# Performance work log

Hardware: AMD Instinct MI355X
Metric: run time of the kernel (lower is better)

Reference implementation:

```python
import jax, jax.numpy as jnp
import numpy as np

V, E, H, L, B, S = 32000, 256, 512, 2, 128, 512


def _lstm_step(x, h, c, w_ih, w_hh, b_ih, b_hh):
    # PyTorch gate order: i, f, g, o
    gates = x @ w_ih.T + b_ih + h @ w_hh.T + b_hh
    i, f, g, o = jnp.split(gates, 4, axis=-1)
    c2 = jax.nn.sigmoid(f) * c + jax.nn.sigmoid(i) * jnp.tanh(g)
    h2 = jax.nn.sigmoid(o) * jnp.tanh(c2)
    return h2, c2


def setup_inputs() -> dict:
    key = jax.random.key(0)
    ks = jax.random.split(key, 16)
    s = 0.05
    d = {}
    d["dec_input"] = jax.random.randint(ks[0], (B,), 0, V)
    d["hidden"] = jax.random.normal(ks[1], (L, B, H), jnp.float32)
    d["cell"] = jax.random.normal(ks[2], (L, B, H), jnp.float32)
    d["encoder_outputs"] = jax.random.normal(ks[3], (S, B, H), jnp.float32)
    d["emb"] = jax.random.normal(ks[4], (V, E), jnp.float32) * s
    d["attn_w"] = jax.random.normal(ks[5], (1, 2 * H), jnp.float32) * s
    d["attn_b"] = jnp.zeros((1,), jnp.float32)
    d["w_ih0"] = jax.random.normal(ks[6], (4 * H, E + H), jnp.float32) * s
    d["w_hh0"] = jax.random.normal(ks[7], (4 * H, H), jnp.float32) * s
    d["b_ih0"] = jnp.zeros((4 * H,), jnp.float32)
    d["b_hh0"] = jnp.zeros((4 * H,), jnp.float32)
    d["w_ih1"] = jax.random.normal(ks[8], (4 * H, H), jnp.float32) * s
    d["w_hh1"] = jax.random.normal(ks[9], (4 * H, H), jnp.float32) * s
    d["b_ih1"] = jnp.zeros((4 * H,), jnp.float32)
    d["b_hh1"] = jnp.zeros((4 * H,), jnp.float32)
    d["fc_w"] = jax.random.normal(ks[10], (V, H), jnp.float32) * s
    d["fc_b"] = jnp.zeros((V,), jnp.float32)
    return d


def reference(dec_input, hidden, cell, encoder_outputs, emb, attn_w, attn_b,
              w_ih0, w_hh0, b_ih0, b_hh0, w_ih1, w_hh1, b_ih1, b_hh1,
              fc_w, fc_b):
    # embedded: [B, E]  (dropout p=0 -> identity)
    embedded = emb[dec_input]
    # Bahdanau-style additive scoring using FIRST-layer hidden (as in source)
    h0 = hidden[0]                                   # [B, H]
    w_enc, w_hid = attn_w[0, :H], attn_w[0, H:]      # split linear over concat
    # logits[b,s] = enc[s,b]@w_enc + h0[b]@w_hid + b
    logits = jnp.einsum('sbh,h->bs', encoder_outputs, w_enc) \
        + (h0 @ w_hid)[:, None] + attn_b[0]          # [B, S]
    alpha = jax.nn.softmax(logits, axis=1)           # softmax over src positions
    # context = sum_s alpha[b,s] * enc[s,b,:]  (avoids repeat_interleave blowup)
    context = jnp.einsum('bs,sbh->bh', alpha, encoder_outputs)  # [B, H]
    x = jnp.concatenate([context, embedded], axis=1)            # [B, H+E]
    # single-timestep 2-layer LSTM
    h_0, c_0 = _lstm_step(x, hidden[0], cell[0], w_ih0, w_hh0, b_ih0, b_hh0)
    h_1, c_1 = _lstm_step(h_0, hidden[1], cell[1], w_ih1, w_hh1, b_ih1, b_hh1)
    new_hidden = jnp.stack([h_0, h_1])
    new_cell = jnp.stack([c_0, c_1])
    prediction = h_1 @ fc_w.T + fc_b                 # [B, V]
    return prediction, new_hidden, new_cell
```

## Files before the change

### kernel.cpp

```cpp
#include <hip/hip_runtime.h>
#include <hip/hip_bf16.h>
#include <math.h>

constexpr int NV = 32000;
constexpr int NE = 256;
constexpr int NH = 512;
constexpr int NB = 128;
constexpr int NS = 512;
constexpr int NX = NH + NE;
constexpr int NSC = 8;

typedef __attribute__((ext_vector_type(8))) short short8;
typedef __attribute__((ext_vector_type(4))) short short4v;
typedef __attribute__((ext_vector_type(4))) float f32x4;

constexpr size_t OFF_PCTX  = 0;
constexpr size_t OFF_PML   = OFF_PCTX  + (size_t)NB*NSC*NH;
constexpr size_t OFF_XBF   = OFF_PML   + (size_t)NB*NSC*2;
constexpr size_t OFF_H0NBF = OFF_XBF   + 49152;
constexpr size_t OFF_H1NBF = OFF_H0NBF + 32768;
constexpr size_t OFF_H0BFI = OFF_H1NBF + 32768;
constexpr size_t OFF_H1BFI = OFF_H0BFI + 32768;

constexpr size_t OUT_HID  = (size_t)NB * NV;
constexpr size_t OUT_CELL = OUT_HID + 2ull * NB * NH;

__device__ inline float sigf(float x) { return 1.0f / (1.0f + expf(-x)); }
__device__ inline short bf16s(float x) {
  __hip_bfloat16 h = __float2bfloat16(x);
  return *reinterpret_cast<short*>(&h);
}

__global__ __launch_bounds__(256) void attn_partial_k(
    const float* __restrict__ enc, const float* __restrict__ attn_w,
    float* __restrict__ pctx, float* __restrict__ pml) {
  const int sc = blockIdx.x, b = blockIdx.y;
  const int wv = threadIdx.x >> 6, lane = threadIdx.x & 63;
  const f32x4 wa = *reinterpret_cast<const f32x4*>(attn_w + lane * 4);
  const f32x4 wb = *reinterpret_cast<const f32x4*>(attn_w + 256 + lane * 4);
  float m0 = -INFINITY, l0 = 0.f, m1 = -INFINITY, l1 = 0.f;
  f32x4 a00 = {}, a01 = {}, a10 = {}, a11 = {};
  const float* base = enc + ((size_t)(sc * 64 + wv) * NB + b) * NH;
  for (int i = 0; i < 8; ++i) {
    const float* r0 = base + (size_t)(i * 4) * NB * NH;
    const float* r1 = base + (size_t)((i + 8) * 4) * NB * NH;
    f32x4 e00 = *reinterpret_cast<const f32x4*>(r0 + lane * 4);
    f32x4 e01 = *reinterpret_cast<const f32x4*>(r0 + 256 + lane * 4);
    f32x4 e10 = *reinterpret_cast<const f32x4*>(r1 + lane * 4);
    f32x4 e11 = *reinterpret_cast<const f32x4*>(r1 + 256 + lane * 4);
    float d0 = e00.x * wa.x + e00.y * wa.y + e00.z * wa.z + e00.w * wa.w
             + e01.x * wb.x + e01.y * wb.y + e01.z * wb.z + e01.w * wb.w;
    float d1 = e10.x * wa.x + e10.y * wa.y + e10.z * wa.z + e10.w * wa.w
             + e11.x * wb.x + e11.y * wb.y + e11.z * wb.z + e11.w * wb.w;
#pragma unroll
    for (int off = 32; off; off >>= 1) {
      d0 += __shfl_xor(d0, off);
      d1 += __shfl_xor(d1, off);
    }
    float mn0 = fmaxf(m0, d0), mn1 = fmaxf(m1, d1);
    float s0 = expf(m0 - mn0), s1 = expf(m1 - mn1);
    float p0 = expf(d0 - mn0), p1 = expf(d1 - mn1);
    l0 = l0 * s0 + p0;         l1 = l1 * s1 + p1;
    a00 = a00 * s0 + p0 * e00; a01 = a01 * s0 + p0 * e01;
    a10 = a10 * s1 + p1 * e10; a11 = a11 * s1 + p1 * e11;
    m0 = mn0; m1 = mn1;
  }
  const float Mw = fmaxf(m0, m1);
  const float c0 = expf(m0 - Mw), c1 = expf(m1 - Mw);
  const float lw = l0 * c0 + l1 * c1;
  const f32x4 accA = a00 * c0 + a10 * c1;
  const f32x4 accB = a01 * c0 + a11 * c1;
  __shared__ float sm[4], sl[4], sacc[4][NH];
  if (lane == 0) { sm[wv] = Mw; sl[wv] = lw; }
  *reinterpret_cast<f32x4*>(&sacc[wv][lane * 4]) = accA;
  *reinterpret_cast<f32x4*>(&sacc[wv][256 + lane * 4]) = accB;
  __syncthreads();
  const float M = fmaxf(fmaxf(sm[0], sm[1]), fmaxf(sm[2], sm[3]));
  const float e0 = expf(sm[0] - M), e1 = expf(sm[1] - M),
              e2 = expf(sm[2] - M), e3 = expf(sm[3] - M);
  const int t = threadIdx.x;
  float* outc = pctx + ((size_t)b * NSC + sc) * NH;
#pragma unroll
  for (int q = 0; q < 2; ++q) {
    int h = q * 256 + t;
    outc[h] = sacc[0][h] * e0 + sacc[1][h] * e1 + sacc[2][h] * e2 + sacc[3][h] * e3;
  }
  if (t == 0) {
    pml[((size_t)b * NSC + sc) * 2 + 0] = M;
    pml[((size_t)b * NSC + sc) * 2 + 1] = sl[0] * e0 + sl[1] * e1 + sl[2] * e2 + sl[3] * e3;
  }
}

__global__ __launch_bounds__(256) void attn_finish_k(
    const float* __restrict__ pctx, const float* __restrict__ pml,
    const float* __restrict__ emb, const int* __restrict__ dec,
    const float* __restrict__ hidden,
    __hip_bfloat16* __restrict__ xbf,
    __hip_bfloat16* __restrict__ h0bf, __hip_bfloat16* __restrict__ h1bf) {
  const int b = blockIdx.x, t = threadIdx.x;
  float ms[NSC];
  float M = -INFINITY;
#pragma unroll
  for (int sc = 0; sc < NSC; ++sc) {
    ms[sc] = pml[((size_t)b * NSC + sc) * 2 + 0];
    M = fmaxf(M, ms[sc]);
  }
  float L = 0.f, es[NSC];
#pragma unroll
  for (int sc = 0; sc < NSC; ++sc) {
    es[sc] = expf(ms[sc] - M);
    L += pml[((size_t)b * NSC + sc) * 2 + 1] * es[sc];
  }
  const float invL = 1.f / L;
#pragma unroll
  for (int q = 0; q < 2; ++q) {
    int h = q * 256 + t;
    float v = 0.f;
#pragma unroll
    for (int sc = 0; sc < NSC; ++sc)
      v += pctx[((size_t)b * NSC + sc) * NH + h] * es[sc];
    xbf[(size_t)b * NX + h] = __float2bfloat16(v * invL);
    h0bf[(size_t)b * NH + h] = __float2bfloat16(hidden[(size_t)b * NH + h]);
    h1bf[(size_t)b * NH + h] =
        __float2bfloat16(hidden[(size_t)(NB * NH) + (size_t)b * NH + h]);
  }
  xbf[(size_t)b * NX + NH + t] = __float2bfloat16(emb[(size_t)dec[b] * NE + t]);
}

constexpr int LSLAB = 520;
template <int KX>
__global__ __launch_bounds__(128, 2) void lstm_fused_k(
    const float* __restrict__ Wx, const float* __restrict__ Wh,
    const __hip_bfloat16* __restrict__ Ax, const __hip_bfloat16* __restrict__ Ah,
    const float* __restrict__ b_ih, const float* __restrict__ b_hh,
    const float* __restrict__ c_in,
    float* __restrict__ h_out, float* __restrict__ c_out,
    __hip_bfloat16* __restrict__ hbf_out) {
  constexpr int NCHX = KX / 256;
  constexpr int NCH = NCHX + 2;
  __shared__ short wlds[2][8 * LSLAB];
  __shared__ float sg[32][17];
  const int tid = threadIdx.x, wv = tid >> 6, lane = tid & 63;
  const int l15 = lane & 15, lhi = lane >> 4;
  const int mh = blockIdx.x, p = blockIdx.y;
  const int srow = tid >> 6;
  const int scol = lane * 4;
  const int soff0 = (scol >> 5) * LSLAB + (scol & 31);
  const int arow = mh * 32 + wv * 16 + l15;

  short8 afbuf[2][8];
  f32x4 wr[8];

#define A_LOAD(c, buf)                                                        \
  {                                                                           \
    const __hip_bfloat16* ab =                                                \
        ((c) < NCHX) ? (Ax + (size_t)arow * KX + (c) * 256 + lhi * 8)         \
                     : (Ah + (size_t)arow * NH + ((c) - NCHX) * 256 + lhi * 8);\
    _Pragma("unroll")                                                         \
    for (int ks = 0; ks < 8; ++ks)                                            \
      (buf)[ks] = *reinterpret_cast<const short8*>(ab + ks * 32);             \
  }
#define LSTAGE_LOAD(c)                                                        \
  {                                                                           \
    const bool fx = (c) < NCHX;                                               \
    const float* Ws = fx ? Wx : Wh;                                           \
    const int Ks = fx ? KX : NH;                                              \
    const int cb = fx ? (c) * 256 : ((c) - NCHX) * 256;                       \
    _Pragma("unroll")                                                         \
    for (int i = 0; i < 8; ++i) {                                             \
      const int j = i * 2 + srow;                                             \
      const int g = j >> 2, rr = j & 3;                                       \
      wr[i] = *reinterpret_cast<const f32x4*>(                                \
          Ws + (size_t)(g * NH + p * 4 + rr) * Ks + cb + scol);               \
    }                                                                         \
  }
#define LSTAGE_WRITE(buf)                                                     \
  {                                                                           \
    _Pragma("unroll")                                                         \
    for (int i = 0; i < 8; ++i) {                                             \
      const int j = i * 2 + srow;                                             \
      short4v cv;                                                             \
      cv[0] = bf16s(wr[i].x); cv[1] = bf16s(wr[i].y);                         \
      cv[2] = bf16s(wr[i].z); cv[3] = bf16s(wr[i].w);                         \
      *reinterpret_cast<short4v*>((buf) + soff0 + j * 32) = cv;               \
    }                                                                         \
  }

  A_LOAD(0, afbuf[0]);
  LSTAGE_LOAD(0);
  LSTAGE_WRITE(wlds[0]);
  __syncthreads();

  f32x4 acc = {};
#pragma unroll
  for (int c = 0; c < NCH; ++c) {
    if (c + 1 < NCH) {
      LSTAGE_LOAD(c + 1);
      A_LOAD(c + 1, afbuf[(c + 1) & 1]);
    }
    {
      const short* wb = wlds[c & 1];
#pragma unroll
      for (int ks = 0; ks < 8; ++ks) {
        short8 bf = *reinterpret_cast<const short8*>(wb + ks * LSLAB + l15 * 32 + lhi * 8);
        acc = __builtin_amdgcn_mfma_f32_16x16x32_bf16(afbuf[c & 1][ks], bf, acc, 0, 0, 0);
      }
    }
    if (c + 1 < NCH) {
      LSTAGE_WRITE(wlds[(c + 1) & 1]);
      __syncthreads();
    }
  }
#pragma unroll
  for (int q = 0; q < 4; ++q)
    sg[wv * 16 + lhi * 4 + q][l15] = acc[q];
  __syncthreads();
  {
    const int bl = tid >> 2, r = tid & 3;
    const int b = mh * 32 + bl;
    const int h = p * 4 + r;
    float ig = sg[bl][0 + r]  + b_ih[0 * NH + h] + b_hh[0 * NH + h];
    float fg = sg[bl][4 + r]  + b_ih[1 * NH + h] + b_hh[1 * NH + h];
    float gg = sg[bl][8 + r]  + b_ih[2 * NH + h] + b_hh[2 * NH + h];
    float og = sg[bl][12 + r] + b_ih[3 * NH + h] + b_hh[3 * NH + h];
    float c = c_in[(size_t)b * NH + h];
    float c2 = sigf(fg) * c + sigf(ig) * tanhf(gg);
    float h2 = sigf(og) * tanhf(c2);
    c_out[(size_t)b * NH + h] = c2;
    h_out[(size_t)b * NH + h] = h2;
    hbf_out[(size_t)b * NH + h] = __float2bfloat16(h2);
  }
#undef A_LOAD
#undef LSTAGE_LOAD
#undef LSTAGE_WRITE
}

constexpr int FC_PANELS = 8;
constexpr int FC_BLOCKS = NV / (16 * FC_PANELS);
constexpr int SLAB = 520;

__global__ __launch_bounds__(256, 1) void gemm_fc_pipe_k(
    const __hip_bfloat16* __restrict__ Abf, const float* __restrict__ W,
    const float* __restrict__ bias, float* __restrict__ out) {
  __shared__ short wlds[2][16 * SLAB];
  const int tid = threadIdx.x, wv = tid >> 6, lane = tid & 63;
  const int l15 = lane & 15, lhi = lane >> 4;
  const int nbase = blockIdx.x * (16 * FC_PANELS);

  int soff[8];
#pragma unroll
  for (int i = 0; i < 8; ++i) {
    const int o = i * 1024 + tid * 4;
    const int n = o >> 9, kk = o & 511;
    soff[i] = (kk >> 5) * SLAB + n * 32 + (kk & 31);
  }

  short8 af[2][16];
#pragma unroll
  for (int m = 0; m < 2; ++m) {
    const __hip_bfloat16* ar = Abf + (size_t)(wv * 32 + m * 16 + l15) * NH + lhi * 8;
#pragma unroll
    for (int ks = 0; ks < 16; ++ks)
      af[m][ks] = *reinterpret_cast<const short8*>(ar + ks * 32);
  }

  f32x4 wr[8];
  {
    const float* panel = W + (size_t)nbase * NH;
#pragma unroll
    for (int i = 0; i < 8; ++i)
      wr[i] = *reinterpret_cast<const f32x4*>(panel + i * 1024 + tid * 4);
    short* wb0 = wlds[0];
#pragma unroll
    for (int i = 0; i < 8; ++i) {
      short4v cv;
      cv[0] = bf16s(wr[i].x); cv[1] = bf16s(wr[i].y);
      cv[2] = bf16s(wr[i].z); cv[3] = bf16s(wr[i].w);
      *reinterpret_cast<short4v*>(wb0 + soff[i]) = cv;
    }
  }
  __syncthreads();

  f32x4 s0 = {}, s1 = {};
  int sn0 = -1;
  for (int p = 0; p < FC_PANELS; ++p) {
    if (p < FC_PANELS - 1) {
      const float* panel = W + (size_t)(nbase + (p + 1) * 16) * NH;
#pragma unroll
      for (int i = 0; i < 8; ++i)
        wr[i] = *reinterpret_cast<const f32x4*>(panel + i * 1024 + tid * 4);
    }
    if (sn0 >= 0) {
      const float bv = bias[sn0 + l15];
#pragma unroll
      for (int q = 0; q < 4; ++q) {
        out[(size_t)(wv * 32 + 0 * 16 + lhi * 4 + q) * NV + sn0 + l15] = s0[q] + bv;
        out[(size_t)(wv * 32 + 1 * 16 + lhi * 4 + q) * NV + sn0 + l15] = s1[q] + bv;
      }
    }
    {
      const short* wb = wlds[p & 1];
      f32x4 a0 = {}, a1 = {};
#pragma unroll
      for (int ks = 0; ks < 16; ++ks) {
        short8 bf = *reinterpret_cast<const short8*>(wb + ks * SLAB + l15 * 32 + lhi * 8);
        a0 = __builtin_amdgcn_mfma_f32_16x16x32_bf16(af[0][ks], bf, a0, 0, 0, 0);
        a1 = __builtin_amdgcn_mfma_f32_16x16x32_bf16(af[1][ks], bf, a1, 0, 0, 0);
      }
      s0 = a0; s1 = a1; sn0 = nbase + p * 16;
    }
    if (p < FC_PANELS - 1) {
      short* wbn = wlds[(p + 1) & 1];
#pragma unroll
      for (int i = 0; i < 8; ++i) {
        short4v cv;
        cv[0] = bf16s(wr[i].x); cv[1] = bf16s(wr[i].y);
        cv[2] = bf16s(wr[i].z); cv[3] = bf16s(wr[i].w);
        *reinterpret_cast<short4v*>(wbn + soff[i]) = cv;
      }
      __syncthreads();
    }
  }
  {
    const float bv = bias[sn0 + l15];
#pragma unroll
    for (int q = 0; q < 4; ++q) {
      out[(size_t)(wv * 32 + 0 * 16 + lhi * 4 + q) * NV + sn0 + l15] = s0[q] + bv;
      out[(size_t)(wv * 32 + 1 * 16 + lhi * 4 + q) * NV + sn0 + l15] = s1[q] + bv;
    }
  }
}

extern "C" void kernel_launch(void* const* d_in, const int* in_sizes, int n_in,
                              void* d_out, int out_size, void* d_ws, size_t ws_size,
                              hipStream_t stream) {
  const int*   dec    = (const int*)d_in[0];
  const float* hidden = (const float*)d_in[1];
  const float* cell   = (const float*)d_in[2];
  const float* enc    = (const float*)d_in[3];
  const float* emb    = (const float*)d_in[4];
  const float* attn_w = (const float*)d_in[5];
  const float* w_ih0  = (const float*)d_in[7];
  const float* w_hh0  = (const float*)d_in[8];
  const float* b_ih0  = (const float*)d_in[9];
  const float* b_hh0  = (const float*)d_in[10];
  const float* w_ih1  = (const float*)d_in[11];
  const float* w_hh1  = (const float*)d_in[12];
  const float* b_ih1  = (const float*)d_in[13];
  const float* b_hh1  = (const float*)d_in[14];
  const float* fc_w   = (const float*)d_in[15];
  const float* fc_b   = (const float*)d_in[16];
  float* out = (float*)d_out;
  float* ws  = (float*)d_ws;

  float* pctx = ws + OFF_PCTX;
  float* pml  = ws + OFF_PML;
  __hip_bfloat16* xbf   = (__hip_bfloat16*)(ws + OFF_XBF);
  __hip_bfloat16* h0nbf = (__hip_bfloat16*)(ws + OFF_H0NBF);
  __hip_bfloat16* h1nbf = (__hip_bfloat16*)(ws + OFF_H1NBF);
  __hip_bfloat16* h0bf  = (__hip_bfloat16*)(ws + OFF_H0BFI);
  __hip_bfloat16* h1bf  = (__hip_bfloat16*)(ws + OFF_H1BFI);

  attn_partial_k<<<dim3(NSC, NB), 256, 0, stream>>>(enc, attn_w, pctx, pml);
  attn_finish_k<<<NB, 256, 0, stream>>>(pctx, pml, emb, dec, hidden,
                                        xbf, h0bf, h1bf);
  lstm_fused_k<NX><<<dim3(4, NH / 4), 128, 0, stream>>>(
      w_ih0, w_hh0, xbf, h0bf, b_ih0, b_hh0, cell,
      out + OUT_HID, out + OUT_CELL, h0nbf);
  lstm_fused_k<NH><<<dim3(4, NH / 4), 128, 0, stream>>>(
      w_ih1, w_hh1, h0nbf, h1bf, b_ih1, b_hh1, cell + NB * NH,
      out + OUT_HID + (size_t)NB * NH,
      out + OUT_CELL + (size_t)NB * NH, h1nbf);
  gemm_fc_pipe_k<<<FC_BLOCKS, 256, 0, stream>>>(h1nbf, fc_w, fc_b, out);
}
```

Before: 66.40 us.

## Deepen FC weight pipeline to two panels ahead with triple-buffered LDS

The fc GEMM kernel now prefetches weight panels two iterations ahead into a double register buffer and uses three LDS slabs. Panel p+1 is converted and written to LDS before the MFMA work on panel p, which leaves one barrier per iteration. The loop is fully unrolled so the register buffer indices are fixed at compile time. The aim is to hide more global-load latency on the weight stream. The cost is more registers (another 8 float4) and more LDS, with one block per CU already set by the launch bounds.

```diff
diff --git a/kernel.cpp b/kernel.cpp
--- a/kernel.cpp
+++ b/kernel.cpp
@@ -242,7 +242,7 @@
 __global__ __launch_bounds__(256, 1) void gemm_fc_pipe_k(
     const __hip_bfloat16* __restrict__ Abf, const float* __restrict__ W,
     const float* __restrict__ bias, float* __restrict__ out) {
-  __shared__ short wlds[2][16 * SLAB];
+  __shared__ short wlds[3][16 * SLAB];
   const int tid = threadIdx.x, wv = tid >> 6, lane = tid & 63;
   const int l15 = lane & 15, lhi = lane >> 4;
   const int nbase = blockIdx.x * (16 * FC_PANELS);
@@ -264,31 +264,35 @@
       af[m][ks] = *reinterpret_cast<const short8*>(ar + ks * 32);
   }
 
-  f32x4 wr[8];
+  f32x4 wrb[2][8];
   {
-    const float* panel = W + (size_t)nbase * NH;
+    const float* p0 = W + (size_t)nbase * NH;
 #pragma unroll
     for (int i = 0; i < 8; ++i)
-      wr[i] = *reinterpret_cast<const f32x4*>(panel + i * 1024 + tid * 4);
-    short* wb0 = wlds[0];
+      wrb[0][i] = *reinterpret_cast<const f32x4*>(p0 + i * 1024 + tid * 4);
+    const float* p1 = W + (size_t)(nbase + 16) * NH;
+#pragma unroll
+    for (int i = 0; i < 8; ++i)
+      wrb[1][i] = *reinterpret_cast<const f32x4*>(p1 + i * 1024 + tid * 4);
 #pragma unroll
     for (int i = 0; i < 8; ++i) {
       short4v cv;
-      cv[0] = bf16s(wr[i].x); cv[1] = bf16s(wr[i].y);
-      cv[2] = bf16s(wr[i].z); cv[3] = bf16s(wr[i].w);
-      *reinterpret_cast<short4v*>(wb0 + soff[i]) = cv;
+      cv[0] = bf16s(wrb[0][i].x); cv[1] = bf16s(wrb[0][i].y);
+      cv[2] = bf16s(wrb[0][i].z); cv[3] = bf16s(wrb[0][i].w);
+      *reinterpret_cast<short4v*>(wlds[0] + soff[i]) = cv;
     }
   }
   __syncthreads();
 
   f32x4 s0 = {}, s1 = {};
   int sn0 = -1;
+#pragma unroll
   for (int p = 0; p < FC_PANELS; ++p) {
-    if (p < FC_PANELS - 1) {
-      const float* panel = W + (size_t)(nbase + (p + 1) * 16) * NH;
+    if (p + 2 < FC_PANELS) {
+      const float* pan = W + (size_t)(nbase + (p + 2) * 16) * NH;
 #pragma unroll
       for (int i = 0; i < 8; ++i)
-        wr[i] = *reinterpret_cast<const f32x4*>(panel + i * 1024 + tid * 4);
+        wrb[p & 1][i] = *reinterpret_cast<const f32x4*>(pan + i * 1024 + tid * 4);
     }
     if (sn0 >= 0) {
       const float bv = bias[sn0 + l15];
@@ -298,8 +302,18 @@
         out[(size_t)(wv * 32 + 1 * 16 + lhi * 4 + q) * NV + sn0 + l15] = s1[q] + bv;
       }
     }
+    if (p + 1 < FC_PANELS) {
+      short* dst = wlds[(p + 1) % 3];
+#pragma unroll
+      for (int i = 0; i < 8; ++i) {
+        short4v cv;
+        cv[0] = bf16s(wrb[(p + 1) & 1][i].x); cv[1] = bf16s(wrb[(p + 1) & 1][i].y);
+        cv[2] = bf16s(wrb[(p + 1) & 1][i].z); cv[3] = bf16s(wrb[(p + 1) & 1][i].w);
+        *reinterpret_cast<short4v*>(dst + soff[i]) = cv;
+      }
+    }
     {
-      const short* wb = wlds[p & 1];
+      const short* wb = wlds[p % 3];
       f32x4 a0 = {}, a1 = {};
 #pragma unroll
       for (int ks = 0; ks < 16; ++ks) {
@@ -309,17 +323,7 @@
       }
       s0 = a0; s1 = a1; sn0 = nbase + p * 16;
     }
-    if (p < FC_PANELS - 1) {
-      short* wbn = wlds[(p + 1) & 1];
-#pragma unroll
-      for (int i = 0; i < 8; ++i) {
-        short4v cv;
-        cv[0] = bf16s(wr[i].x); cv[1] = bf16s(wr[i].y);
-        cv[2] = bf16s(wr[i].z); cv[3] = bf16s(wr[i].w);
-        *reinterpret_cast<short4v*>(wbn + soff[i]) = cv;
-      }
-      __syncthreads();
-    }
+    __syncthreads();
   }
   {
     const float bv = bias[sn0 + l15];
```

Result: no change. 65.56 us (-1.3%).
